# Kernel optimization log

Hardware: AMD Instinct MI355X
Metric: run time of the kernel (lower is better)

## Reference

```python
import jax, jax.numpy as jnp
import numpy as np
from jax import lax

EMB_DIM = 16
NUM_EMB = 32
DN = ('NCDHW', 'OIDHW', 'NCDHW')


def conv3d(x, w, b, stride, pad):
    y = lax.conv_general_dilated(x, w, window_strides=(stride,) * 3,
                                 padding=[(pad, pad)] * 3, dimension_numbers=DN)
    return y + b[None, :, None, None, None]


def deconv3d(x, w, b, stride, pad):
    # PyTorch ConvTranspose3d: weight (Cin,Cout,k,k,k); equivalent to conv with
    # spatially flipped, channel-transposed kernel, lhs_dilation=stride, pad=k-1-p.
    k = w.shape[-1]
    wf = jnp.flip(w, axis=(2, 3, 4)).transpose(1, 0, 2, 3, 4)  # (Cout,Cin,k,k,k)
    y = lax.conv_general_dilated(x, wf, window_strides=(1, 1, 1),
                                 padding=[(k - 1 - pad, k - 1 - pad)] * 3,
                                 lhs_dilation=(stride,) * 3, dimension_numbers=DN)
    return y + b[None, :, None, None, None]


def setup_inputs() -> dict:
    key = jax.random.key(0)
    ks = jax.random.split(key, 16)
    x = jax.random.normal(ks[0], (16, 3, 16, 128, 128), dtype=jnp.float32)
    s = 0.05
    # encoder params
    enc_w1 = jax.random.normal(ks[1], (4, 3, 4, 4, 4), jnp.float32) * s
    enc_b1 = jnp.zeros((4,), jnp.float32)
    enc_w2 = jax.random.normal(ks[2], (8, 4, 4, 4, 4), jnp.float32) * s
    enc_b2 = jnp.zeros((8,), jnp.float32)
    enc_w4 = jax.random.normal(ks[3], (EMB_DIM, 8, 3, 3, 3), jnp.float32) * s
    enc_b4 = jnp.zeros((EMB_DIM,), jnp.float32)
    # decoder params (ConvTranspose3d layout: (Cin, Cout, k, k, k))
    dec_w1 = jax.random.normal(ks[4], (EMB_DIM, 8, 4, 4, 4), jnp.float32) * s
    dec_b1 = jnp.zeros((8,), jnp.float32)
    dec_w3 = jax.random.normal(ks[5], (8, 4, 4, 4, 4), jnp.float32) * s
    dec_b3 = jnp.zeros((4,), jnp.float32)
    dec_w4 = jax.random.normal(ks[6], (4, 3, 3, 3, 3), jnp.float32) * s
    dec_b4 = jnp.zeros((3,), jnp.float32)
    # codebook buffers: normalize(randn)*0.1, rows 0/1 forced
    e = jax.random.normal(ks[7], (NUM_EMB, EMB_DIM), jnp.float32)
    e = e / jnp.linalg.norm(e, axis=1, keepdims=True) * 0.1
    embedding = e.at[0].set(0.0).at[1].set(6.0)
    cluster_size = jnp.ones((NUM_EMB,), jnp.float32)
    return dict(x=x, epoch=60,
                enc_w1=enc_w1, enc_b1=enc_b1, enc_w2=enc_w2, enc_b2=enc_b2,
                enc_w4=enc_w4, enc_b4=enc_b4,
                dec_w1=dec_w1, dec_b1=dec_b1, dec_w3=dec_w3, dec_b3=dec_b3,
                dec_w4=dec_w4, dec_b4=dec_b4,
                embedding=embedding, cluster_size=cluster_size)


def reference(x, epoch, enc_w1, enc_b1, enc_w2, enc_b2, enc_w4, enc_b4,
              dec_w1, dec_b1, dec_w3, dec_b3, dec_w4, dec_b4,
              embedding, cluster_size):
    # ---- Encoder ----
    h = jax.nn.relu(conv3d(x, enc_w1, enc_b1, 2, 1))
    h = jax.nn.relu(conv3d(h, enc_w2, enc_b2, 2, 1))
    z = jnp.clip(conv3d(h, enc_w4, enc_b4, 1, 1), 0.0, 6.0)  # relu(relu6(.))
    B, C, Dd, Hh, Ww = z.shape

    # ---- VQ-EMA forward (epoch >= 50 branch) ----
    emb = embedding.at[0].set(0.0).at[1].set(6.0)
    flat = z.transpose(0, 2, 3, 4, 1).reshape(-1, C)  # (N, D)
    # squared euclidean distances; argmin matches cdist argmin
    d2 = (jnp.sum(flat * flat, axis=1, keepdims=True)
          - 2.0 * flat @ emb.T + jnp.sum(emb * emb, axis=1))
    idx = jnp.argmin(d2, axis=1)                       # (N,)
    q = emb[idx]                                       # (N, D)
    quant = q.reshape(B, Dd, Hh, Ww, C).transpose(0, 4, 1, 2, 3)

    N = flat.shape[0]
    avg_probs = jnp.zeros((NUM_EMB,), flat.dtype).at[idx].add(1.0) / N
    perplexity = jnp.exp(-jnp.sum(avg_probs * jnp.log(avg_probs + 1e-10)))
    used_codes = jnp.sum(cluster_size > 1e-5).astype(jnp.float32) / NUM_EMB

    quantized_st = z + lax.stop_gradient(quant - z)
    vq_loss = 0.25 * jnp.mean((lax.stop_gradient(quant) - z) ** 2)
    codes = idx.reshape(B, Dd, Hh, Ww)

    # ---- Decoder ----
    d = jax.nn.relu(deconv3d(quantized_st, dec_w1, dec_b1, 2, 1))
    d = jax.nn.relu(deconv3d(d, dec_w3, dec_b3, 2, 1))
    out = deconv3d(d, dec_w4, dec_b4, 1, 1)
    return out, vq_loss, codes, perplexity, used_codes
```

## Files before the change

kernel.cpp:

```cpp
#include <hip/hip_runtime.h>
#include <math.h>

#define NB 16


__device__ __forceinline__ float4 ld4(const float* p) {
  return *reinterpret_cast<const float4*>(p);
}
__device__ __forceinline__ void st4(float* p, float4 v) {
  *reinterpret_cast<float4*>(p) = v;
}

__global__ __launch_bounds__(256) void conv1_k(
    const float* __restrict__ x, const float* __restrict__ w,
    const float* __restrict__ bias, float* __restrict__ y) {
  int idx = blockIdx.x * 256 + threadIdx.x;
  int g  = idx & 15;
  int oh = (idx >> 4) & 63;
  int od = (idx >> 10) & 7;
  int n  = idx >> 13;
  bool gl = (g > 0), gr = (g < 15);
  float acc[4][4];
  #pragma unroll
  for (int co = 0; co < 4; co++) {
    float bv = bias[co];
    #pragma unroll
    for (int m = 0; m < 4; m++) acc[co][m] = bv;
  }
  int ih0 = 2 * oh - 1;
  #pragma unroll 1
  for (int ci = 0; ci < 3; ci++) {
    #pragma unroll 1
    for (int kd = 0; kd < 4; kd++) {
      int id = 2 * od - 1 + kd;
      bool vd = (unsigned)id < 16u;
      int idc = vd ? id : 0;
      const float* plane = x + (((n * 3 + ci) * 16 + idc) * 16384);
      #pragma unroll
      for (int kh = 0; kh < 4; kh++) {
        int ih = ih0 + kh;
        bool v = vd && ((unsigned)ih < 128u);
        int ihc = (unsigned)ih < 128u ? ih : 0;
        const float* rp = plane + ihc * 128 + 8 * g;
        float r[10];
        float4 A = ld4(rp);
        float4 B = ld4(rp + 4);
        float rl = rp[-1 * (int)gl];
        float rr = rp[gr ? 8 : 0];
        r[0] = (v && gl) ? rl : 0.0f;
        r[1] = v ? A.x : 0.0f; r[2] = v ? A.y : 0.0f;
        r[3] = v ? A.z : 0.0f; r[4] = v ? A.w : 0.0f;
        r[5] = v ? B.x : 0.0f; r[6] = v ? B.y : 0.0f;
        r[7] = v ? B.z : 0.0f; r[8] = v ? B.w : 0.0f;
        r[9] = (v && gr) ? rr : 0.0f;
        #pragma unroll
        for (int co = 0; co < 4; co++) {
          const float* wb = w + ((co * 3 + ci) * 4 + kd) * 16 + kh * 4;
          #pragma unroll
          for (int kw = 0; kw < 4; kw++) {
            float wv = wb[kw];
            #pragma unroll
            for (int m = 0; m < 4; m++)
              acc[co][m] += r[2 * m + kw] * wv;
          }
        }
      }
    }
  }
  #pragma unroll
  for (int co = 0; co < 4; co++) {
    float4 o;
    o.x = fmaxf(acc[co][0], 0.0f); o.y = fmaxf(acc[co][1], 0.0f);
    o.z = fmaxf(acc[co][2], 0.0f); o.w = fmaxf(acc[co][3], 0.0f);
    st4(y + ((n * 4 + co) * 8 + od) * 4096 + oh * 64 + 4 * g, o);
  }
}

__global__ __launch_bounds__(256) void conv2_k(
    const float* __restrict__ y1, const float* __restrict__ w,
    const float* __restrict__ bias, float* __restrict__ y) {
  int idx = blockIdx.x * 256 + threadIdx.x;
  int ow = idx & 31;
  int oh = (idx >> 5) & 31;
  int od = (idx >> 10) & 3;
  int n = (idx >> 12) & 15;
  int cog = idx >> 16;
  float acc[4];
  #pragma unroll
  for (int co = 0; co < 4; co++) acc[co] = bias[cog * 4 + co];
  int id0 = 2 * od - 1, ih0 = 2 * oh - 1, iw0 = 2 * ow - 1;
  bool vh[4], vw[4];
  #pragma unroll
  for (int l = 0; l < 4; l++) {
    vh[l] = (unsigned)(ih0 + l) < 64u;
    vw[l] = (unsigned)(iw0 + l) < 64u;
  }
  #pragma unroll 1
  for (int ci = 0; ci < 4; ci++) {
    const float* ip = y1 + ((n * 4 + ci) * 8) * 4096;
    #pragma unroll
    for (int kd = 0; kd < 4; kd++) {
      int id = id0 + kd;
      bool vd = (unsigned)id < 8u;
      const float* pp = ip + id * 4096;
      float p[4][4];
      #pragma unroll
      for (int kh = 0; kh < 4; kh++)
        #pragma unroll
        for (int kw = 0; kw < 4; kw++)
          p[kh][kw] = (vd && vh[kh] && vw[kw]) ? pp[(ih0 + kh) * 64 + (iw0 + kw)] : 0.0f;
      #pragma unroll
      for (int co = 0; co < 4; co++) {
        const float* wp = w + (((cog * 4 + co) * 4 + ci) * 4 + kd) * 16;
        #pragma unroll
        for (int kh = 0; kh < 4; kh++)
          #pragma unroll
          for (int kw = 0; kw < 4; kw++)
            acc[co] += p[kh][kw] * wp[kh * 4 + kw];
      }
    }
  }
  #pragma unroll
  for (int co = 0; co < 4; co++)
    y[((n * 8 + cog * 4 + co) * 4 + od) * 1024 + oh * 32 + ow] = fmaxf(acc[co], 0.0f);
}

__global__ __launch_bounds__(256) void conv4_k(
    const float* __restrict__ y2, const float* __restrict__ w,
    const float* __restrict__ bias, float* __restrict__ z) {
  int idx = blockIdx.x * 256 + threadIdx.x;
  int ow = idx & 31;
  int oh = (idx >> 5) & 31;
  int od = (idx >> 10) & 3;
  int n = (idx >> 12) & 15;
  int cog = idx >> 16;
  float acc[4];
  #pragma unroll
  for (int co = 0; co < 4; co++) acc[co] = bias[cog * 4 + co];
  bool vh[3], vw[3];
  #pragma unroll
  for (int l = 0; l < 3; l++) {
    vh[l] = (unsigned)(oh - 1 + l) < 32u;
    vw[l] = (unsigned)(ow - 1 + l) < 32u;
  }
  #pragma unroll 1
  for (int ci = 0; ci < 8; ci++) {
    const float* ip = y2 + ((n * 8 + ci) * 4) * 1024;
    #pragma unroll
    for (int kd = 0; kd < 3; kd++) {
      int id = od - 1 + kd;
      bool vd = (unsigned)id < 4u;
      const float* pp = ip + id * 1024;
      float p[3][3];
      #pragma unroll
      for (int kh = 0; kh < 3; kh++)
        #pragma unroll
        for (int kw = 0; kw < 3; kw++)
          p[kh][kw] = (vd && vh[kh] && vw[kw]) ? pp[(oh - 1 + kh) * 32 + (ow - 1 + kw)] : 0.0f;
      #pragma unroll
      for (int co = 0; co < 4; co++) {
        const float* wp = w + (((cog * 4 + co) * 8 + ci) * 3 + kd) * 9;
        #pragma unroll
        for (int kh = 0; kh < 3; kh++)
          #pragma unroll
          for (int kw = 0; kw < 3; kw++)
            acc[co] += p[kh][kw] * wp[kh * 3 + kw];
      }
    }
  }
  #pragma unroll
  for (int co = 0; co < 4; co++)
    z[((n * 16 + cog * 4 + co) * 4 + od) * 1024 + oh * 32 + ow] =
        fminf(fmaxf(acc[co], 0.0f), 6.0f);
}

__global__ __launch_bounds__(256) void vq_k(
    const float* __restrict__ z, const float* __restrict__ emb,
    float* __restrict__ quant, float* __restrict__ codes_out,
    float* __restrict__ stats) {
  __shared__ float se[32 * 16];
  __shared__ float se2[32];
  __shared__ float shist[32];
  __shared__ float swred[4];
  int tid = threadIdx.x;
  for (int i = tid; i < 512; i += 256) {
    int r = i >> 4;
    float v = emb[i];
    if (r == 0) v = 0.0f;
    else if (r == 1) v = 6.0f;
    se[i] = v;
  }
  if (tid < 32) shist[tid] = 0.0f;
  __syncthreads();
  if (tid < 32) {
    float s = 0.0f;
    #pragma unroll
    for (int d = 0; d < 16; d++) { float v = se[tid * 16 + d]; s += v * v; }
    se2[tid] = s;
  }
  __syncthreads();

  int idx = blockIdx.x * 256 + tid;
  float lsum = 0.0f;
  {
    int w_ = idx & 31; int t = idx >> 5;
    int h_ = t & 31; t >>= 5;
    int d_ = t & 3;  int b_ = t >> 2;
    const float* zp = z + b_ * 65536 + d_ * 1024 + h_ * 32 + w_;
    float f[16];
    float f2 = 0.0f;
    #pragma unroll
    for (int c = 0; c < 16; c++) { float v = zp[c * 4096]; f[c] = v; f2 += v * v; }
    float best = 1e30f; int bi = 0;
    for (int e = 0; e < 32; e++) {
      float dot = 0.0f;
      #pragma unroll
      for (int c = 0; c < 16; c++) dot += f[c] * se[e * 16 + c];
      float d2 = f2 - 2.0f * dot + se2[e];
      if (d2 < best) { best = d2; bi = e; }
    }
    float* qp = quant + b_ * 65536 + d_ * 1024 + h_ * 32 + w_;
    #pragma unroll
    for (int c = 0; c < 16; c++) {
      float q = se[bi * 16 + c];
      qp[c * 4096] = q;
      float df = q - f[c];
      lsum += df * df;
    }
    codes_out[idx] = (float)bi;
    atomicAdd(&shist[bi], 1.0f);
  }
  for (int o = 32; o; o >>= 1) lsum += __shfl_down(lsum, o);
  if ((tid & 63) == 0) swred[tid >> 6] = lsum;
  __syncthreads();
  if (tid == 0) atomicAdd(&stats[0], swred[0] + swred[1] + swred[2] + swred[3]);
  if (tid < 32) {
    float h = shist[tid];
    if (h != 0.0f) atomicAdd(&stats[1 + tid], h);
  }
}

__global__ void init_stats_k(float* __restrict__ stats) {
  int tid = threadIdx.x;
  if (tid < 33) stats[tid] = 0.0f;
}

__global__ void fin_k(const float* __restrict__ stats,
                      const float* __restrict__ cluster_size,
                      float* __restrict__ out_loss, float* __restrict__ out_perp,
                      float* __restrict__ out_used) {
  int tid = threadIdx.x;
  float v = 0.0f;
  float used = 0.0f;
  if (tid < 32) {
    float p = stats[1 + tid] * (1.0f / 65536.0f);
    v = p * logf(p + 1e-10f);
    used = (cluster_size[tid] > 1e-5f) ? 1.0f : 0.0f;
  }
  for (int o = 16; o; o >>= 1) { v += __shfl_down(v, o); used += __shfl_down(used, o); }
  if (tid == 0) {
    *out_perp = expf(-v);
    *out_used = used * (1.0f / 32.0f);
    *out_loss = 0.25f * stats[0] * (1.0f / 1048576.0f);
  }
}

__global__ __launch_bounds__(256) void deconv1_k(
    const float* __restrict__ q, const float* __restrict__ w,
    const float* __restrict__ bias, float* __restrict__ d1) {
  int bid = blockIdx.x;
  int cog = bid & 1;
  int ph  = (bid >> 1) & 1;
  int od  = (bid >> 2) & 7;
  int n   = bid >> 5;
  int tid = threadIdx.x;
  int g   = tid & 7;
  int bl  = tid >> 3;
  bool glf = (g > 0), grf = (g < 7);

  int kd0 = (od + 1) & 1;
  int idtop = (od + 1 - kd0) >> 1;
  int kh0 = (ph + 1) & 1;
  int ihtop = bl + ph;

  float acc[4][8];
  #pragma unroll
  for (int co = 0; co < 4; co++) {
    float bv = bias[cog * 4 + co];
    #pragma unroll
    for (int m = 0; m < 8; m++) acc[co][m] = bv;
  }

  #pragma unroll 1
  for (int ci = 0; ci < 16; ci++) {
    const float* ip = q + ((n * 16 + ci) * 4) * 1024;
    #pragma unroll
    for (int jd = 0; jd < 2; jd++) {
      int id = idtop - jd;
      bool vd = (unsigned)id < 4u;
      int idc = vd ? id : 0;
      const float* plane = ip + idc * 1024;
      #pragma unroll
      for (int jh = 0; jh < 2; jh++) {
        int ih = ihtop - jh;
        bool v = vd && ((unsigned)ih < 32u);
        int ihc = (unsigned)ih < 32u ? ih : 0;
        const float* rp = plane + ihc * 32 + 4 * g;
        float r[6];
        float4 A = ld4(rp);
        float rl = rp[-1 * (int)glf];
        float rr = rp[grf ? 4 : 0];
        r[0] = (v && glf) ? rl : 0.0f;
        r[1] = v ? A.x : 0.0f; r[2] = v ? A.y : 0.0f;
        r[3] = v ? A.z : 0.0f; r[4] = v ? A.w : 0.0f;
        r[5] = (v && grf) ? rr : 0.0f;
        int kd = kd0 + 2 * jd;
        int kh = kh0 + 2 * jh;
        #pragma unroll
        for (int co = 0; co < 4; co++) {
          const float* wb = w + ((ci * 8 + cog * 4 + co) * 4 + kd) * 16 + kh * 4;
          #pragma unroll
          for (int jw = 0; jw < 2; jw++) {
            float w_ev = wb[1 + 2 * jw];
            float w_od = wb[2 * jw];
            #pragma unroll
            for (int ii = 0; ii < 4; ii++) {
              acc[co][2 * ii]     += r[ii + 1 - jw] * w_ev;
              acc[co][2 * ii + 1] += r[ii + 2 - jw] * w_od;
            }
          }
        }
      }
    }
  }
  int oh = 2 * bl + ph;
  #pragma unroll
  for (int co = 0; co < 4; co++) {
    float* op = d1 + ((n * 8 + cog * 4 + co) * 8 + od) * 4096 + oh * 64 + 8 * g;
    float4 lo, hi;
    lo.x = fmaxf(acc[co][0], 0.0f); lo.y = fmaxf(acc[co][1], 0.0f);
    lo.z = fmaxf(acc[co][2], 0.0f); lo.w = fmaxf(acc[co][3], 0.0f);
    hi.x = fmaxf(acc[co][4], 0.0f); hi.y = fmaxf(acc[co][5], 0.0f);
    hi.z = fmaxf(acc[co][6], 0.0f); hi.w = fmaxf(acc[co][7], 0.0f);
    st4(op, lo); st4(op + 4, hi);
  }
}

__global__ __launch_bounds__(256) void deconv3_k(
    const float* __restrict__ d1, const float* __restrict__ w,
    const float* __restrict__ bias, float* __restrict__ d2) {
  const int KD[2][2] = {{1, 3}, {0, 2}};
  const int LI[2][2] = {{1, 0}, {2, 1}};
  int idx = blockIdx.x * 256 + threadIdx.x;
  int c = idx & 63;
  int b = (idx >> 6) & 63;
  int a = (idx >> 12) & 7;
  int n = idx >> 15;
  float acc[2][2][2][4];
  #pragma unroll
  for (int pd = 0; pd < 2; pd++)
    #pragma unroll
    for (int ph = 0; ph < 2; ph++)
      #pragma unroll
      for (int pw = 0; pw < 2; pw++)
        #pragma unroll
        for (int co = 0; co < 4; co++) acc[pd][ph][pw][co] = bias[co];
  bool vd[3], vh[3], vw[3];
  #pragma unroll
  for (int l = 0; l < 3; l++) {
    vd[l] = (unsigned)(a - 1 + l) < 8u;
    vh[l] = (unsigned)(b - 1 + l) < 64u;
    vw[l] = (unsigned)(c - 1 + l) < 64u;
  }
  #pragma unroll 1
  for (int ci = 0; ci < 8; ci++) {
    const float* ip = d1 + ((n * 8 + ci) * 8) * 4096;
    float in[3][3][3];
    #pragma unroll
    for (int ld = 0; ld < 3; ld++)
      #pragma unroll
      for (int lh = 0; lh < 3; lh++)
        #pragma unroll
        for (int lw = 0; lw < 3; lw++)
          in[ld][lh][lw] = (vd[ld] && vh[lh] && vw[lw])
              ? ip[(a - 1 + ld) * 4096 + (b - 1 + lh) * 64 + (c - 1 + lw)] : 0.0f;
    #pragma unroll
    for (int pd = 0; pd < 2; pd++)
      #pragma unroll
      for (int jd = 0; jd < 2; jd++) {
        int kd = KD[pd][jd], ld = LI[pd][jd];
        #pragma unroll
        for (int ph = 0; ph < 2; ph++)
          #pragma unroll
          for (int jh = 0; jh < 2; jh++) {
            int kh = KD[ph][jh], lh = LI[ph][jh];
            #pragma unroll
            for (int pw = 0; pw < 2; pw++)
              #pragma unroll
              for (int jw = 0; jw < 2; jw++) {
                int kw = KD[pw][jw], lw = LI[pw][jw];
                float iv = in[ld][lh][lw];
                #pragma unroll
                for (int co = 0; co < 4; co++)
                  acc[pd][ph][pw][co] +=
                      iv * w[((ci * 4 + co) * 4 + kd) * 16 + kh * 4 + kw];
              }
          }
      }
  }
  #pragma unroll
  for (int co = 0; co < 4; co++)
    #pragma unroll
    for (int pd = 0; pd < 2; pd++)
      #pragma unroll
      for (int ph = 0; ph < 2; ph++)
        #pragma unroll
        for (int pw = 0; pw < 2; pw++)
          d2[((n * 4 + co) * 16 + 2 * a + pd) * 16384 +
             (2 * b + ph) * 128 + (2 * c + pw)] = fmaxf(acc[pd][ph][pw][co], 0.0f);
}

__global__ __launch_bounds__(256) void deconv4_k(
    const float* __restrict__ d2, const float* __restrict__ w,
    const float* __restrict__ bias, float* __restrict__ out) {
  int idx = blockIdx.x * 256 + threadIdx.x;
  int c = idx & 63;
  int b = (idx >> 6) & 63;
  int a = (idx >> 12) & 7;
  int n = idx >> 15;
  float acc[2][2][2][3];
  #pragma unroll
  for (int pd = 0; pd < 2; pd++)
    #pragma unroll
    for (int ph = 0; ph < 2; ph++)
      #pragma unroll
      for (int pw = 0; pw < 2; pw++)
        #pragma unroll
        for (int co = 0; co < 3; co++) acc[pd][ph][pw][co] = bias[co];
  int ih0 = 2 * b - 1, iw0 = 2 * c - 1;
  bool vh[4], vw[4];
  #pragma unroll
  for (int l = 0; l < 4; l++) {
    vh[l] = (unsigned)(ih0 + l) < 128u;
    vw[l] = (unsigned)(iw0 + l) < 128u;
  }
  #pragma unroll 1
  for (int ci = 0; ci < 4; ci++) {
    const float* ip = d2 + ((n * 4 + ci) * 16) * 16384;
    #pragma unroll
    for (int ld = 0; ld < 4; ld++) {
      int id = 2 * a - 1 + ld;
      bool vdl = (unsigned)id < 16u;
      const float* pp = ip + id * 16384;
      float p[4][4];
      #pragma unroll
      for (int lh = 0; lh < 4; lh++)
        #pragma unroll
        for (int lw = 0; lw < 4; lw++)
          p[lh][lw] = (vdl && vh[lh] && vw[lw]) ? pp[(ih0 + lh) * 128 + (iw0 + lw)] : 0.0f;
      #pragma unroll
      for (int pd = 0; pd < 2; pd++) {
        int kd = pd + 2 - ld;
        if (kd < 0 || kd > 2) continue;
        #pragma unroll
        for (int kh = 0; kh < 3; kh++)
          #pragma unroll
          for (int kw = 0; kw < 3; kw++)
            #pragma unroll
            for (int co = 0; co < 3; co++) {
              float wv = w[(ci * 3 + co) * 27 + kd * 9 + kh * 3 + kw];
              #pragma unroll
              for (int ph = 0; ph < 2; ph++)
                #pragma unroll
                for (int pw = 0; pw < 2; pw++)
                  acc[pd][ph][pw][co] += p[ph + 2 - kh][pw + 2 - kw] * wv;
            }
      }
    }
  }
  #pragma unroll
  for (int co = 0; co < 3; co++)
    #pragma unroll
    for (int pd = 0; pd < 2; pd++)
      #pragma unroll
      for (int ph = 0; ph < 2; ph++)
        #pragma unroll
        for (int pw = 0; pw < 2; pw++)
          out[((n * 3 + co) * 16 + 2 * a + pd) * 16384 +
              (2 * b + ph) * 128 + (2 * c + pw)] = acc[pd][ph][pw][co];
}

extern "C" void kernel_launch(void* const* d_in, const int* in_sizes, int n_in,
                              void* d_out, int out_size, void* d_ws, size_t ws_size,
                              hipStream_t stream) {
  const float* x      = (const float*)d_in[0];
  const float* enc_w1 = (const float*)d_in[2];
  const float* enc_b1 = (const float*)d_in[3];
  const float* enc_w2 = (const float*)d_in[4];
  const float* enc_b2 = (const float*)d_in[5];
  const float* enc_w4 = (const float*)d_in[6];
  const float* enc_b4 = (const float*)d_in[7];
  const float* dec_w1 = (const float*)d_in[8];
  const float* dec_b1 = (const float*)d_in[9];
  const float* dec_w3 = (const float*)d_in[10];
  const float* dec_b3 = (const float*)d_in[11];
  const float* dec_w4 = (const float*)d_in[12];
  const float* dec_b4 = (const float*)d_in[13];
  const float* emb    = (const float*)d_in[14];
  const float* csize  = (const float*)d_in[15];

  float* ws = (float*)d_ws;
  float* stats = ws;
  float* quant = ws + 64;
  float* z     = quant + 1048576;
  float* y2    = z + 1048576;
  float* y1    = y2 + 524288;
  float* d1    = z;
  float* d2    = ws + 64 + 1048576 + 4194304;

  float* out   = (float*)d_out;
  float* out_loss  = out + 12582912;
  float* out_codes = out_loss + 1;
  float* out_perp  = out_codes + 65536;
  float* out_used  = out_perp + 1;

  init_stats_k<<<1, 64, 0, stream>>>(stats);

  conv1_k<<<512, 256, 0, stream>>>(x, enc_w1, enc_b1, y1);
  conv2_k<<<512, 256, 0, stream>>>(y1, enc_w2, enc_b2, y2);
  conv4_k<<<1024, 256, 0, stream>>>(y2, enc_w4, enc_b4, z);

  vq_k<<<256, 256, 0, stream>>>(z, emb, quant, out_codes, stats);
  fin_k<<<1, 64, 0, stream>>>(stats, csize, out_loss, out_perp, out_used);

  deconv1_k<<<512, 256, 0, stream>>>(quant, dec_w1, dec_b1, d1);
  deconv3_k<<<2048, 256, 0, stream>>>(d1, dec_w3, dec_b3, d2);
  deconv4_k<<<2048, 256, 0, stream>>>(d2, dec_w4, dec_b4, out);
}
```

Baseline: 387.5 us.

## Restructure deconv3 and deconv4 into row-strip threads with vectorized loads and stores

Both decoder transposed-conv kernels now assign each thread an 8-wide strip of one output row instead of a 2x2x2 parity cube. Input rows are read as float4 loads plus two halo scalars, and the results go out as two float4 stores. This replaces scattered strided stride-2 scalar stores and many scalar gathers with coalesced vector memory traffic, and it uses only the taps valid for each output parity. In exchange, neighbouring threads read overlapping halo elements, and each thread keeps more accumulators in registers.

Measured after the change: 399.2 us. 3.0% more time.

```diff
diff --git a/kernel.cpp b/kernel.cpp
--- a/kernel.cpp
+++ b/kernel.cpp
@@ -349,145 +349,150 @@
 __global__ __launch_bounds__(256) void deconv3_k(
     const float* __restrict__ d1, const float* __restrict__ w,
     const float* __restrict__ bias, float* __restrict__ d2) {
-  const int KD[2][2] = {{1, 3}, {0, 2}};
-  const int LI[2][2] = {{1, 0}, {2, 1}};
-  int idx = blockIdx.x * 256 + threadIdx.x;
-  int c = idx & 63;
-  int b = (idx >> 6) & 63;
-  int a = (idx >> 12) & 7;
-  int n = idx >> 15;
-  float acc[2][2][2][4];
-  #pragma unroll
-  for (int pd = 0; pd < 2; pd++)
-    #pragma unroll
-    for (int ph = 0; ph < 2; ph++)
-      #pragma unroll
-      for (int pw = 0; pw < 2; pw++)
-        #pragma unroll
-        for (int co = 0; co < 4; co++) acc[pd][ph][pw][co] = bias[co];
-  bool vd[3], vh[3], vw[3];
-  #pragma unroll
-  for (int l = 0; l < 3; l++) {
-    vd[l] = (unsigned)(a - 1 + l) < 8u;
-    vh[l] = (unsigned)(b - 1 + l) < 64u;
-    vw[l] = (unsigned)(c - 1 + l) < 64u;
-  }
+  int bid = blockIdx.x;
+  int ph  = bid & 1;
+  int blh = (bid >> 1) & 3;
+  int od  = (bid >> 3) & 15;
+  int n   = bid >> 7;
+  int tid = threadIdx.x;
+  int g   = tid & 15;
+  int bl  = tid >> 4;
+  int BL  = blh * 16 + bl;
+  bool glf = (g > 0), grf = (g < 15);
+
+  int kd0 = (od + 1) & 1;
+  int idtop = (od + 1 - kd0) >> 1;
+  int kh0 = (ph + 1) & 1;
+  int ihtop = BL + ph;
+
+  float acc[4][8];
+  #pragma unroll
+  for (int co = 0; co < 4; co++) {
+    float bv = bias[co];
+    #pragma unroll
+    for (int m = 0; m < 8; m++) acc[co][m] = bv;
+  }
+
   #pragma unroll 1
   for (int ci = 0; ci < 8; ci++) {
     const float* ip = d1 + ((n * 8 + ci) * 8) * 4096;
-    float in[3][3][3];
-    #pragma unroll
-    for (int ld = 0; ld < 3; ld++)
-      #pragma unroll
-      for (int lh = 0; lh < 3; lh++)
-        #pragma unroll
-        for (int lw = 0; lw < 3; lw++)
-          in[ld][lh][lw] = (vd[ld] && vh[lh] && vw[lw])
-              ? ip[(a - 1 + ld) * 4096 + (b - 1 + lh) * 64 + (c - 1 + lw)] : 0.0f;
-    #pragma unroll
-    for (int pd = 0; pd < 2; pd++)
-      #pragma unroll
-      for (int jd = 0; jd < 2; jd++) {
-        int kd = KD[pd][jd], ld = LI[pd][jd];
-        #pragma unroll
-        for (int ph = 0; ph < 2; ph++)
+    #pragma unroll
+    for (int jd = 0; jd < 2; jd++) {
+      int id = idtop - jd;
+      bool vd = (unsigned)id < 8u;
+      int idc = vd ? id : 0;
+      const float* plane = ip + idc * 4096;
+      #pragma unroll
+      for (int jh = 0; jh < 2; jh++) {
+        int ih = ihtop - jh;
+        bool v = vd && ((unsigned)ih < 64u);
+        int ihc = (unsigned)ih < 64u ? ih : 0;
+        const float* rp = plane + ihc * 64 + 4 * g;
+        float r[6];
+        float4 A = ld4(rp);
+        float rl = rp[-1 * (int)glf];
+        float rr = rp[grf ? 4 : 0];
+        r[0] = (v && glf) ? rl : 0.0f;
+        r[1] = v ? A.x : 0.0f; r[2] = v ? A.y : 0.0f;
+        r[3] = v ? A.z : 0.0f; r[4] = v ? A.w : 0.0f;
+        r[5] = (v && grf) ? rr : 0.0f;
+        int kd = kd0 + 2 * jd;
+        int kh = kh0 + 2 * jh;
+        #pragma unroll
+        for (int co = 0; co < 4; co++) {
+          const float* wb = w + ((ci * 4 + co) * 4 + kd) * 16 + kh * 4;
           #pragma unroll
-          for (int jh = 0; jh < 2; jh++) {
-            int kh = KD[ph][jh], lh = LI[ph][jh];
+          for (int jw = 0; jw < 2; jw++) {
+            float w_ev = wb[1 + 2 * jw];
+            float w_od = wb[2 * jw];
             #pragma unroll
-            for (int pw = 0; pw < 2; pw++)
-              #pragma unroll
-              for (int jw = 0; jw < 2; jw++) {
-                int kw = KD[pw][jw], lw = LI[pw][jw];
-                float iv = in[ld][lh][lw];
-                #pragma unroll
-                for (int co = 0; co < 4; co++)
-                  acc[pd][ph][pw][co] +=
-                      iv * w[((ci * 4 + co) * 4 + kd) * 16 + kh * 4 + kw];
-              }
+            for (int ii = 0; ii < 4; ii++) {
+              acc[co][2 * ii]     += r[ii + 1 - jw] * w_ev;
+              acc[co][2 * ii + 1] += r[ii + 2 - jw] * w_od;
+            }
           }
+        }
       }
-  }
-  #pragma unroll
-  for (int co = 0; co < 4; co++)
-    #pragma unroll
-    for (int pd = 0; pd < 2; pd++)
-      #pragma unroll
-      for (int ph = 0; ph < 2; ph++)
-        #pragma unroll
-        for (int pw = 0; pw < 2; pw++)
-          d2[((n * 4 + co) * 16 + 2 * a + pd) * 16384 +
-             (2 * b + ph) * 128 + (2 * c + pw)] = fmaxf(acc[pd][ph][pw][co], 0.0f);
+    }
+  }
+  int oh = 2 * BL + ph;
+  #pragma unroll
+  for (int co = 0; co < 4; co++) {
+    float* op = d2 + ((n * 4 + co) * 16 + od) * 16384 + oh * 128 + 8 * g;
+    float4 lo, hi;
+    lo.x = fmaxf(acc[co][0], 0.0f); lo.y = fmaxf(acc[co][1], 0.0f);
+    lo.z = fmaxf(acc[co][2], 0.0f); lo.w = fmaxf(acc[co][3], 0.0f);
+    hi.x = fmaxf(acc[co][4], 0.0f); hi.y = fmaxf(acc[co][5], 0.0f);
+    hi.z = fmaxf(acc[co][6], 0.0f); hi.w = fmaxf(acc[co][7], 0.0f);
+    st4(op, lo); st4(op + 4, hi);
+  }
 }
 
 __global__ __launch_bounds__(256) void deconv4_k(
     const float* __restrict__ d2, const float* __restrict__ w,
     const float* __restrict__ bias, float* __restrict__ out) {
   int idx = blockIdx.x * 256 + threadIdx.x;
-  int c = idx & 63;
-  int b = (idx >> 6) & 63;
-  int a = (idx >> 12) & 7;
-  int n = idx >> 15;
-  float acc[2][2][2][3];
-  #pragma unroll
-  for (int pd = 0; pd < 2; pd++)
-    #pragma unroll
-    for (int ph = 0; ph < 2; ph++)
-      #pragma unroll
-      for (int pw = 0; pw < 2; pw++)
-        #pragma unroll
-        for (int co = 0; co < 3; co++) acc[pd][ph][pw][co] = bias[co];
-  int ih0 = 2 * b - 1, iw0 = 2 * c - 1;
-  bool vh[4], vw[4];
-  #pragma unroll
-  for (int l = 0; l < 4; l++) {
-    vh[l] = (unsigned)(ih0 + l) < 128u;
-    vw[l] = (unsigned)(iw0 + l) < 128u;
-  }
+  int g  = idx & 15;
+  int oh = (idx >> 4) & 127;
+  int od = (idx >> 11) & 15;
+  int n  = idx >> 15;
+  bool gl = (g > 0), gr = (g < 15);
+  float acc[3][8];
+  #pragma unroll
+  for (int co = 0; co < 3; co++) {
+    float bv = bias[co];
+    #pragma unroll
+    for (int m = 0; m < 8; m++) acc[co][m] = bv;
+  }
+  int ih0 = oh - 1;
   #pragma unroll 1
   for (int ci = 0; ci < 4; ci++) {
     const float* ip = d2 + ((n * 4 + ci) * 16) * 16384;
     #pragma unroll
-    for (int ld = 0; ld < 4; ld++) {
-      int id = 2 * a - 1 + ld;
-      bool vdl = (unsigned)id < 16u;
-      const float* pp = ip + id * 16384;
-      float p[4][4];
-      #pragma unroll
-      for (int lh = 0; lh < 4; lh++)
-        #pragma unroll
-        for (int lw = 0; lw < 4; lw++)
-          p[lh][lw] = (vdl && vh[lh] && vw[lw]) ? pp[(ih0 + lh) * 128 + (iw0 + lw)] : 0.0f;
-      #pragma unroll
-      for (int pd = 0; pd < 2; pd++) {
-        int kd = pd + 2 - ld;
-        if (kd < 0 || kd > 2) continue;
-        #pragma unroll
-        for (int kh = 0; kh < 3; kh++)
+    for (int kd = 0; kd < 3; kd++) {
+      int id = od - 1 + kd;
+      bool vd = (unsigned)id < 16u;
+      int idc = vd ? id : 0;
+      const float* plane = ip + idc * 16384;
+      #pragma unroll
+      for (int kh = 0; kh < 3; kh++) {
+        int ih = ih0 + kh;
+        bool v = vd && ((unsigned)ih < 128u);
+        int ihc = (unsigned)ih < 128u ? ih : 0;
+        const float* rp = plane + ihc * 128 + 8 * g;
+        float r[10];
+        float4 A = ld4(rp);
+        float4 B = ld4(rp + 4);
+        float rl = rp[-1 * (int)gl];
+        float rr = rp[gr ? 8 : 0];
+        r[0] = (v && gl) ? rl : 0.0f;
+        r[1] = v ? A.x : 0.0f; r[2] = v ? A.y : 0.0f;
+        r[3] = v ? A.z : 0.0f; r[4] = v ? A.w : 0.0f;
+        r[5] = v ? B.x : 0.0f; r[6] = v ? B.y : 0.0f;
+        r[7] = v ? B.z : 0.0f; r[8] = v ? B.w : 0.0f;
+        r[9] = (v && gr) ? rr : 0.0f;
+        #pragma unroll
+        for (int co = 0; co < 3; co++) {
+          const float* wb = w + (ci * 3 + co) * 27 + (2 - kd) * 9 + (2 - kh) * 3 + 2;
           #pragma unroll
-          for (int kw = 0; kw < 3; kw++)
+          for (int kw = 0; kw < 3; kw++) {
+            float wv = wb[-kw];
             #pragma unroll
-            for (int co = 0; co < 3; co++) {
-              float wv = w[(ci * 3 + co) * 27 + kd * 9 + kh * 3 + kw];
-              #pragma unroll
-              for (int ph = 0; ph < 2; ph++)
-                #pragma unroll
-                for (int pw = 0; pw < 2; pw++)
-                  acc[pd][ph][pw][co] += p[ph + 2 - kh][pw + 2 - kw] * wv;
-            }
+            for (int m = 0; m < 8; m++)
+              acc[co][m] += r[m + kw] * wv;
+          }
+        }
       }
     }
   }
   #pragma unroll
-  for (int co = 0; co < 3; co++)
-    #pragma unroll
-    for (int pd = 0; pd < 2; pd++)
-      #pragma unroll
-      for (int ph = 0; ph < 2; ph++)
-        #pragma unroll
-        for (int pw = 0; pw < 2; pw++)
-          out[((n * 3 + co) * 16 + 2 * a + pd) * 16384 +
-              (2 * b + ph) * 128 + (2 * c + pw)] = acc[pd][ph][pw][co];
+  for (int co = 0; co < 3; co++) {
+    float* op = out + ((n * 3 + co) * 16 + od) * 16384 + oh * 128 + 8 * g;
+    float4 lo, hi;
+    lo.x = acc[co][0]; lo.y = acc[co][1]; lo.z = acc[co][2]; lo.w = acc[co][3];
+    hi.x = acc[co][4]; hi.y = acc[co][5]; hi.z = acc[co][6]; hi.w = acc[co][7];
+    st4(op, lo); st4(op + 4, hi);
+  }
 }
 
 extern "C" void kernel_launch(void* const* d_in, const int* in_sizes, int n_in,
```
